# Kernel tuning notes

Hardware: AMD Instinct MI355X
Metric: run time of the kernel (lower is better)

## Reference

```python
import jax, jax.numpy as jnp
import numpy as np

N = 50000      # nodes
E = 800000     # edges
F = 64         # in_channels == out_channels
ED = 16        # edge_dim
G = 64         # graphs in batch
L = 2          # numLayers
BN_EPS = 1e-5
STD_EPS = 1e-5
AGG_DIM = F * 4 * 3  # 4 aggregators x 3 scalers


def setup_inputs() -> dict:
    key = jax.random.key(0)
    ks = jax.random.split(key, 12)
    r = lambda k, shp, fan: (jax.random.normal(k, shp, jnp.float32) / np.sqrt(fan)).astype(jnp.float32)
    return dict(
        x=jax.random.normal(ks[0], (N, F), jnp.float32),
        edge_attr=jax.random.normal(ks[1], (E, ED), jnp.float32),
        We=r(ks[2], (L, ED, F), ED), be=jnp.zeros((L, F), jnp.float32),
        Wpre=r(ks[3], (L, 3 * F, F), 3 * F), bpre=jnp.zeros((L, F), jnp.float32),
        Wpost=r(ks[4], (L, F + AGG_DIM, F), F + AGG_DIM), bpost=jnp.zeros((L, F), jnp.float32),
        Wlin=r(ks[5], (L, F, F), F), blin=jnp.zeros((L, F), jnp.float32),
        gamma=jnp.ones((L, F), jnp.float32), beta=jnp.zeros((L, F), jnp.float32),
        W1=r(ks[6], (F, 40), F), b1=jnp.zeros((40,), jnp.float32),
        W2=r(ks[7], (40, 1), 40), b2=jnp.zeros((1,), jnp.float32),
        edge_index=jax.random.randint(ks[8], (2, E), 0, N),
        batch=jnp.sort(jax.random.randint(ks[9], (N,), 0, G)),
    )


def _ceal_conv(x, src, dst, edge_attr, We, be, Wpre, bpre, Wpost, bpost, Wlin, blin, deg, amp, att):
    # PNA-style conv, towers=1, pre_layers=post_layers=1
    e = edge_attr @ We + be                                              # [E,F]
    h = jnp.concatenate([x[dst], x[src], e], axis=-1) @ Wpre + bpre      # [E,F]
    degc = jnp.maximum(deg, 1.0)[:, None]
    mean = jax.ops.segment_sum(h, dst, num_segments=N) / degc
    sq = jax.ops.segment_sum(h * h, dst, num_segments=N) / degc
    std = jnp.sqrt(jax.nn.relu(sq - mean * mean) + STD_EPS)
    has = (deg > 0)[:, None]
    mn = jnp.where(has, jax.ops.segment_min(h, dst, num_segments=N), 0.0)
    mx = jnp.where(has, jax.ops.segment_max(h, dst, num_segments=N), 0.0)
    aggs = jnp.concatenate([mean, mn, mx, std], axis=-1)                 # [N,4F]
    scaled = jnp.concatenate([aggs, aggs * amp[:, None], aggs * att[:, None]], axis=-1)  # [N,12F]
    out = jnp.concatenate([x, scaled], axis=-1) @ Wpost + bpost          # [N,F]
    return out @ Wlin + blin


def _bn(x, gamma, beta):
    mu = x.mean(0)
    var = x.var(0)  # biased, as torch BatchNorm training-mode normalization
    return (x - mu) * jax.lax.rsqrt(var + BN_EPS) * gamma + beta


def reference(x, edge_attr, We, be, Wpre, bpre, Wpost, bpost, Wlin, blin,
              gamma, beta, W1, b1, W2, b2, edge_index, batch):
    src, dst = edge_index[0], edge_index[1]
    deg = jax.ops.segment_sum(jnp.ones((E,), jnp.float32), dst, num_segments=N)
    avg_log = jnp.mean(jnp.log(deg + 1.0))
    logd = jnp.log(jnp.maximum(deg, 1.0) + 1.0)
    amp = logd / avg_log
    att = avg_log / logd
    for l in range(L):
        x = _ceal_conv(x, src, dst, edge_attr, We[l], be[l], Wpre[l], bpre[l],
                       Wpost[l], bpost[l], Wlin[l], blin[l], deg, amp, att)
        x = jax.nn.relu(_bn(x, gamma[l], beta[l]))
    cnt = jnp.maximum(jax.ops.segment_sum(jnp.ones((N,), jnp.float32), batch, num_segments=G), 1.0)
    gm = jax.ops.segment_sum(x, batch, num_segments=G) / cnt[:, None]    # global_mean_pool [G,F]
    return jax.nn.relu(gm @ W1 + b1) @ W2 + b2                           # [G,1]
```

## Files before the change

### kernel.cpp

```cpp
#include <hip/hip_runtime.h>
#include <math.h>
#include <float.h>

#define NN 50000
#define EE 800000
#define FF 64
#define EDIM 16
#define GG 64
#define NB64 782
#define NSB 196

typedef short bf16x8 __attribute__((ext_vector_type(8)));
typedef float f32x4 __attribute__((ext_vector_type(4)));

__device__ inline unsigned short bf_rne(float v) {
  unsigned int u = __float_as_uint(v);
  unsigned int r = (u + 0x7FFFu + ((u >> 16) & 1u)) >> 16;
  return (unsigned short)r;
}
__device__ inline float bf_up(unsigned short h) {
  return __uint_as_float(((unsigned int)h) << 16);
}
__device__ inline void split4(float4 v, ushort4& h, ushort4& l) {
  h.x = bf_rne(v.x); h.y = bf_rne(v.y); h.z = bf_rne(v.z); h.w = bf_rne(v.w);
  l.x = bf_rne(v.x - bf_up(h.x));
  l.y = bf_rne(v.y - bf_up(h.y));
  l.z = bf_rne(v.z - bf_up(h.z));
  l.w = bf_rne(v.w - bf_up(h.w));
}
__device__ inline float blo(unsigned int u) { return __uint_as_float(u << 16); }
__device__ inline float bhi(unsigned int u) { return __uint_as_float(u & 0xFFFF0000u); }

__global__ void k_deg(const int* __restrict__ eidx, int* __restrict__ deg) {
  int e = blockIdx.x * 256 + threadIdx.x;
  if (e < EE) atomicAdd(&deg[eidx[EE + e]], 1);
}

__global__ __launch_bounds__(256) void k_scanA(const int* __restrict__ deg, int* __restrict__ offsets,
                                               int* __restrict__ bsum, float* __restrict__ lsum) {
  __shared__ int ws[4];
  __shared__ float lw[4];
  int t = threadIdx.x;
  int lane = t & 63;
  int wv = t >> 6;
  int i = blockIdx.x * 256 + t;
  int v = (i < NN) ? deg[i] : 0;
  float lg = (i < NN) ? logf((float)v + 1.0f) : 0.0f;
  int x = v;
  #pragma unroll
  for (int o = 1; o < 64; o <<= 1) {
    int y = __shfl_up(x, o);
    if (lane >= o) x += y;
  }
  #pragma unroll
  for (int o = 1; o < 64; o <<= 1) lg += __shfl_xor(lg, o);
  if (lane == 63) ws[wv] = x;
  if (lane == 0) lw[wv] = lg;
  __syncthreads();
  int pre = 0;
  for (int k = 0; k < wv; k++) pre += ws[k];
  if (i < NN) offsets[i] = pre + x - v;
  if (t == 0) {
    bsum[blockIdx.x] = ws[0] + ws[1] + ws[2] + ws[3];
    lsum[blockIdx.x] = lw[0] + lw[1] + lw[2] + lw[3];
  }
}

__global__ __launch_bounds__(256) void k_scanB(const int* __restrict__ bsum, const float* __restrict__ lsum,
                                               int* __restrict__ bpref, float* __restrict__ meta,
                                               float* __restrict__ scbA) {
  __shared__ int ws[4];
  __shared__ float lw[4];
  int t = threadIdx.x;
  int lane = t & 63;
  int wv = t >> 6;
  int v = (t < NSB) ? bsum[t] : 0;
  float lg = (t < NSB) ? lsum[t] : 0.0f;
  int x = v;
  #pragma unroll
  for (int o = 1; o < 64; o <<= 1) {
    int y = __shfl_up(x, o);
    if (lane >= o) x += y;
  }
  #pragma unroll
  for (int o = 1; o < 64; o <<= 1) lg += __shfl_xor(lg, o);
  if (lane == 63) ws[wv] = x;
  if (lane == 0) lw[wv] = lg;
  __syncthreads();
  int pre = 0;
  for (int k = 0; k < wv; k++) pre += ws[k];
  if (t < NSB) bpref[t] = pre + x - v;
  if (t == 0) meta[0] = (lw[0] + lw[1] + lw[2] + lw[3]) / (float)NN;
  if (t < 64) { scbA[t] = 1.0f; scbA[64 + t] = 0.0f; }
  if (t == 0) scbA[128] = -FLT_MAX;
}

__global__ __launch_bounds__(256) void k_scanC(int* __restrict__ offsets, const int* __restrict__ bpref,
                                               const int* __restrict__ deg, const float* __restrict__ meta,
                                               float* __restrict__ amp, float* __restrict__ att) {
  int i = blockIdx.x * 256 + threadIdx.x;
  if (i < NN) {
    offsets[i] += bpref[blockIdx.x];
    float d = (float)deg[i];
    float avg = meta[0];
    float logd = logf(fmaxf(d, 1.0f) + 1.0f);
    amp[i] = logd / avg;
    att[i] = avg / logd;
  }
  if (i == 0) offsets[NN] = EE;
}

__global__ void k_scatter(const int* __restrict__ eidx, const int* __restrict__ offsets,
                          int* __restrict__ cursor, int* __restrict__ srcs,
                          const float* __restrict__ eattr, unsigned int* __restrict__ PermEA) {
  int e = blockIdx.x * 256 + threadIdx.x;
  if (e < EE) {
    int s = eidx[e];
    int d = eidx[EE + e];
    int pos = offsets[d] + atomicAdd(&cursor[d], 1);
    srcs[pos] = s;
    const float4* ep = (const float4*)(eattr + (size_t)e * EDIM);
    float4 q0 = ep[0], q1 = ep[1], q2 = ep[2], q3 = ep[3];
    uint4 pa, pb;
    pa.x = (unsigned)bf_rne(q0.x) | ((unsigned)bf_rne(q0.y) << 16);
    pa.y = (unsigned)bf_rne(q0.z) | ((unsigned)bf_rne(q0.w) << 16);
    pa.z = (unsigned)bf_rne(q1.x) | ((unsigned)bf_rne(q1.y) << 16);
    pa.w = (unsigned)bf_rne(q1.z) | ((unsigned)bf_rne(q1.w) << 16);
    pb.x = (unsigned)bf_rne(q2.x) | ((unsigned)bf_rne(q2.y) << 16);
    pb.y = (unsigned)bf_rne(q2.z) | ((unsigned)bf_rne(q2.w) << 16);
    pb.z = (unsigned)bf_rne(q3.x) | ((unsigned)bf_rne(q3.y) << 16);
    pb.w = (unsigned)bf_rne(q3.z) | ((unsigned)bf_rne(q3.w) << 16);
    ((uint4*)PermEA)[(size_t)pos * 2] = pa;
    ((uint4*)PermEA)[(size_t)pos * 2 + 1] = pb;
  }
}

__global__ __launch_bounds__(256) void k_prep2(const float* __restrict__ We, const float* __restrict__ be,
                                               const float* __restrict__ Wpre, const float* __restrict__ bpre,
                                               const float* __restrict__ Wpost, const float* __restrict__ bpost,
                                               const float* __restrict__ Wlin, const float* __restrict__ blin,
                                               unsigned short* __restrict__ MwT_h, unsigned short* __restrict__ MwT_l,
                                               float* __restrict__ bconst,
                                               unsigned short* __restrict__ WcT_h, unsigned short* __restrict__ WcT_l,
                                               unsigned short* __restrict__ WxT_h, unsigned short* __restrict__ WxT_l,
                                               float* __restrict__ bcomb) {
  int id = blockIdx.x * 256 + threadIdx.x;
  if (id < 53248) {
    int k = id >> 6, f = id & 63;
    float a = 0.0f;
    for (int j = 0; j < FF; j++) a += Wpost[(size_t)k * FF + j] * Wlin[j * FF + f];
    unsigned short h = bf_rne(a);
    WcT_h[f * 832 + k] = h;
    WcT_l[f * 832 + k] = bf_rne(a - bf_up(h));
  } else if (id < 61440) {
    int lid = id - 53248;
    int j = lid >> 6, k = lid & 63;
    float v = (j < 64) ? Wpre[k * FF + j] : Wpre[(64 + k) * FF + (j - 64)];
    unsigned short h = bf_rne(v);
    WxT_h[j * 64 + k] = h;
    WxT_l[j * 64 + k] = bf_rne(v - bf_up(h));
  } else if (id < 62464) {
    int lid = id - 61440;
    int k = lid >> 6, f = lid & 63;
    float a = 0.0f;
    for (int j = 0; j < FF; j++) a += We[k * FF + j] * Wpre[(128 + j) * FF + f];
    unsigned short h = bf_rne(a);
    int ct = f & 3, jcol = f >> 2;
    MwT_h[(ct * 16 + jcol) * 16 + k] = h;
    MwT_l[(ct * 16 + jcol) * 16 + k] = bf_rne(a - bf_up(h));
  } else {
    int f = threadIdx.x;
    if (blockIdx.x == 244 && f < 64) {
      float b = bpre[f];
      for (int j = 0; j < FF; j++) b += be[j] * Wpre[(128 + j) * FF + f];
      bconst[f] = b;
      float c = blin[f];
      for (int j = 0; j < FF; j++) c += bpost[j] * Wlin[j * FF + f];
      bcomb[f] = c;
    }
  }
}

__global__ __launch_bounds__(256) void k_xform(const float* __restrict__ x, const float* __restrict__ scb,
                                               const unsigned short* __restrict__ WxT_h,
                                               const unsigned short* __restrict__ WxT_l,
                                               float* __restrict__ Xd, unsigned short* __restrict__ Xs) {
  __shared__ unsigned short Ah[64 * 72], Al[64 * 72];
  int t = threadIdx.x;
  int n0 = blockIdx.x * 64;
  {
    int r = t >> 2, c0 = (t & 3) * 16;
    int n = n0 + r;
    bool rok = n < NN;
    const float4* src = (const float4*)(x + (size_t)n * FF + c0);
    float flr = scb[128];
    #pragma unroll
    for (int c4 = 0; c4 < 4; c4++) {
      float4 v = rok ? src[c4] : make_float4(0.f, 0.f, 0.f, 0.f);
      float4 sc = ((const float4*)scb)[(c0 >> 2) + c4];
      float4 of = ((const float4*)(scb + 64))[(c0 >> 2) + c4];
      v.x = fmaxf(v.x * sc.x + of.x, flr);
      v.y = fmaxf(v.y * sc.y + of.y, flr);
      v.z = fmaxf(v.z * sc.z + of.z, flr);
      v.w = fmaxf(v.w * sc.w + of.w, flr);
      ushort4 h4, l4;
      split4(v, h4, l4);
      *(ushort4*)&Ah[r * 72 + c0 + c4 * 4] = h4;
      *(ushort4*)&Al[r * 72 + c0 + c4 * 4] = l4;
    }
  }
  __syncthreads();
  int lane = t & 63;
  int l15 = lane & 15;
  int quad = lane >> 4;
  int w = __builtin_amdgcn_readfirstlane(t >> 6);
  int rbase = (w & 1) * 32;
  int cbase = (w >> 1) * 64;
  f32x4 acc[2][4];
  #pragma unroll
  for (int rt = 0; rt < 2; rt++)
    #pragma unroll
    for (int ct = 0; ct < 4; ct++) acc[rt][ct] = (f32x4){0.f, 0.f, 0.f, 0.f};

  #pragma unroll
  for (int ks = 0; ks < 2; ks++) {
    bf16x8 a_h[2], a_l[2];
    #pragma unroll
    for (int rt = 0; rt < 2; rt++) {
      int row = rbase + rt * 16 + l15;
      a_h[rt] = *(const bf16x8*)&Ah[row * 72 + ks * 32 + quad * 8];
      a_l[rt] = *(const bf16x8*)&Al[row * 72 + ks * 32 + quad * 8];
    }
    #pragma unroll
    for (int ct = 0; ct < 4; ct++) {
      int col = cbase + ct * 16 + l15;
      bf16x8 b_h = *(const bf16x8*)(WxT_h + (size_t)col * 64 + ks * 32 + quad * 8);
      bf16x8 b_l = *(const bf16x8*)(WxT_l + (size_t)col * 64 + ks * 32 + quad * 8);
      #pragma unroll
      for (int rt = 0; rt < 2; rt++) {
        acc[rt][ct] = __builtin_amdgcn_mfma_f32_16x16x32_bf16(a_h[rt], b_h, acc[rt][ct], 0, 0, 0);
        acc[rt][ct] = __builtin_amdgcn_mfma_f32_16x16x32_bf16(a_h[rt], b_l, acc[rt][ct], 0, 0, 0);
        acc[rt][ct] = __builtin_amdgcn_mfma_f32_16x16x32_bf16(a_l[rt], b_h, acc[rt][ct], 0, 0, 0);
      }
    }
  }
  #pragma unroll
  for (int rt = 0; rt < 2; rt++) {
    #pragma unroll
    for (int ct = 0; ct < 4; ct++) {
      int col = cbase + ct * 16 + l15;
      #pragma unroll
      for (int reg = 0; reg < 4; reg++) {
        int n = n0 + rbase + rt * 16 + quad * 4 + reg;
        if (n < NN) {
          float v = acc[rt][ct][reg];
          if (col < 64) Xd[(size_t)n * FF + col] = v;
          else          Xs[(size_t)n * FF + (col - 64)] = bf_rne(v);
        }
      }
    }
  }
}

__global__ __launch_bounds__(256) void k_agg(const int* __restrict__ srcs, const int* __restrict__ offsets,
                                             const unsigned int* __restrict__ PermEA,
                                             const unsigned short* __restrict__ MwT_h,
                                             const unsigned short* __restrict__ MwT_l,
                                             const float* __restrict__ bconst,
                                             const float* __restrict__ Xd, const unsigned short* __restrict__ Xs,
                                             unsigned short* __restrict__ aggs) {
  int wid = __builtin_amdgcn_readfirstlane(threadIdx.x >> 6);
  int lane = threadIdx.x & 63;
  int l15 = lane & 15;
  int quad = lane >> 4;
  int n = blockIdx.x * 4 + wid;
  if (n >= NN) return;

  bf16x8 bh[4], bl[4];
  #pragma unroll
  for (int ct = 0; ct < 4; ct++) {
    if (quad < 2) {
      bh[ct] = *(const bf16x8*)&MwT_h[(ct * 16 + l15) * 16 + quad * 8];
      bl[ct] = *(const bf16x8*)&MwT_l[(ct * 16 + l15) * 16 + quad * 8];
    } else {
      bh[ct] = (bf16x8){0, 0, 0, 0, 0, 0, 0, 0};
      bl[ct] = (bf16x8){0, 0, 0, 0, 0, 0, 0, 0};
    }
  }

  float4 xd4 = *(const float4*)(Xd + (size_t)n * FF + 4 * l15);
  float4 bc4 = *(const float4*)(bconst + 4 * l15);
  float bas[4] = {xd4.x + bc4.x, xd4.y + bc4.y, xd4.z + bc4.z, xd4.w + bc4.w};

  int o0 = offsets[n], o1 = offsets[n + 1];
  float s[4]  = {0.f, 0.f, 0.f, 0.f};
  float sq[4] = {0.f, 0.f, 0.f, 0.f};
  float mn[4] = {FLT_MAX, FLT_MAX, FLT_MAX, FLT_MAX};
  float mx[4] = {-FLT_MAX, -FLT_MAX, -FLT_MAX, -FLT_MAX};

  for (int base = o0; base < o1; base += 16) {
    bf16x8 af = (bf16x8){0, 0, 0, 0, 0, 0, 0, 0};
    if (quad < 2) af = *(const bf16x8*)(PermEA + (size_t)(base + l15) * 8 + quad * 4);
    f32x4 acc[4];
    #pragma unroll
    for (int ct = 0; ct < 4; ct++) {
      f32x4 a = (f32x4){0.f, 0.f, 0.f, 0.f};
      a = __builtin_amdgcn_mfma_f32_16x16x32_bf16(af, bl[ct], a, 0, 0, 0);
      a = __builtin_amdgcn_mfma_f32_16x16x32_bf16(af, bh[ct], a, 0, 0, 0);
      acc[ct] = a;
    }
    #pragma unroll
    for (int reg = 0; reg < 4; reg++) {
      int e = base + quad * 4 + reg;
      bool valid = e < o1;
      int ec = min(e, o1 - 1);
      int src = srcs[ec];
      ushort4 xs4 = *(const ushort4*)(Xs + (size_t)src * FF + 4 * l15);
      float xf[4] = {bf_up(xs4.x), bf_up(xs4.y), bf_up(xs4.z), bf_up(xs4.w)};
      #pragma unroll
      for (int ct = 0; ct < 4; ct++) {
        float h = bas[ct] + xf[ct] + acc[ct][reg];
        float hv = valid ? h : 0.0f;
        s[ct] += hv;
        sq[ct] = fmaf(hv, hv, sq[ct]);
        float t1 = fminf(mn[ct], h);
        float t2 = fmaxf(mx[ct], h);
        mn[ct] = valid ? t1 : mn[ct];
        mx[ct] = valid ? t2 : mx[ct];
      }
    }
  }

  #pragma unroll
  for (int ct = 0; ct < 4; ct++) {
    s[ct] += __shfl_xor(s[ct], 16);  s[ct] += __shfl_xor(s[ct], 32);
    sq[ct] += __shfl_xor(sq[ct], 16); sq[ct] += __shfl_xor(sq[ct], 32);
    mn[ct] = fminf(mn[ct], __shfl_xor(mn[ct], 16)); mn[ct] = fminf(mn[ct], __shfl_xor(mn[ct], 32));
    mx[ct] = fmaxf(mx[ct], __shfl_xor(mx[ct], 16)); mx[ct] = fmaxf(mx[ct], __shfl_xor(mx[ct], 32));
  }

  float d = (float)(o1 - o0);
  float dc = fmaxf(d, 1.0f);
  float rdc = 1.0f / dc;
  bool has = d > 0.0f;
  ushort4 outv;
  unsigned short ov[4];
  #pragma unroll
  for (int ct = 0; ct < 4; ct++) {
    float mean = s[ct] * rdc;
    float msq = sq[ct] * rdc;
    float sd = sqrtf(fmaxf(msq - mean * mean, 0.0f) + 1e-5f);
    float vmn = has ? mn[ct] : 0.0f;
    float vmx = has ? mx[ct] : 0.0f;
    float val = (quad == 0) ? mean : (quad == 1) ? vmn : (quad == 2) ? vmx : sd;
    ov[ct] = bf_rne(val);
  }
  outv.x = ov[0]; outv.y = ov[1]; outv.z = ov[2]; outv.w = ov[3];
  *(ushort4*)(aggs + (size_t)n * 256 + quad * 64 + 4 * l15) = outv;
}

__global__ __launch_bounds__(256) void k_post(const float* __restrict__ x, const float* __restrict__ scb,
                                              const unsigned short* __restrict__ aggs,
                                              const float* __restrict__ amp, const float* __restrict__ att,
                                              const unsigned short* __restrict__ WcT_h,
                                              const unsigned short* __restrict__ WcT_l,
                                              const float* __restrict__ bcomb,
                                              float* __restrict__ y, float* __restrict__ partials) {
  __shared__ unsigned short Ah[64 * 72], Al[64 * 72];
  __shared__ float red_s[4][32], red_q[4][32];
  int t = threadIdx.x;
  int n0 = blockIdx.x * 64;
  int lane = t & 63;
  int l15 = lane & 15;
  int quad = lane >> 4;
  int w = __builtin_amdgcn_readfirstlane(t >> 6);
  int rbase = (w & 1) * 32;
  int cbase = (w >> 1) * 32;

  {
    int ar = t >> 2;
    int ac0 = (t & 3) * 16;
    int an = n0 + ar;
    bool rok = an < NN;
    const float* xrow = x + (size_t)an * FF;
    float flr = scb[128];
    #pragma unroll
    for (int c4 = 0; c4 < 4; c4++) {
      float4 v = rok ? *(const float4*)(xrow + ac0 + c4 * 4) : make_float4(0.f, 0.f, 0.f, 0.f);
      float4 sc = ((const float4*)scb)[(ac0 >> 2) + c4];
      float4 of = ((const float4*)(scb + 64))[(ac0 >> 2) + c4];
      v.x = fmaxf(v.x * sc.x + of.x, flr);
      v.y = fmaxf(v.y * sc.y + of.y, flr);
      v.z = fmaxf(v.z * sc.z + of.z, flr);
      v.w = fmaxf(v.w * sc.w + of.w, flr);
      ushort4 h4, l4;
      split4(v, h4, l4);
      *(ushort4*)&Ah[ar * 72 + ac0 + c4 * 4] = h4;
      *(ushort4*)&Al[ar * 72 + ac0 + c4 * 4] = l4;
    }
  }
  __syncthreads();

  f32x4 acc[3][2][2];
  #pragma unroll
  for (int s = 0; s < 3; s++)
    #pragma unroll
    for (int rt = 0; rt < 2; rt++)
      #pragma unroll
      for (int ct = 0; ct < 2; ct++) acc[s][rt][ct] = (f32x4){0.f, 0.f, 0.f, 0.f};

  #pragma unroll
  for (int ks = 0; ks < 2; ks++) {
    bf16x8 a_h[2], a_l[2];
    #pragma unroll
    for (int rt = 0; rt < 2; rt++) {
      int row = rbase + rt * 16 + l15;
      a_h[rt] = *(const bf16x8*)&Ah[row * 72 + ks * 32 + quad * 8];
      a_l[rt] = *(const bf16x8*)&Al[row * 72 + ks * 32 + quad * 8];
    }
    #pragma unroll
    for (int ct = 0; ct < 2; ct++) {
      int col = cbase + ct * 16 + l15;
      bf16x8 b_h = *(const bf16x8*)(WcT_h + (size_t)col * 832 + ks * 32 + quad * 8);
      bf16x8 b_l = *(const bf16x8*)(WcT_l + (size_t)col * 832 + ks * 32 + quad * 8);
      #pragma unroll
      for (int rt = 0; rt < 2; rt++) {
        acc[0][rt][ct] = __builtin_amdgcn_mfma_f32_16x16x32_bf16(a_h[rt], b_h, acc[0][rt][ct], 0, 0, 0);
        acc[0][rt][ct] = __builtin_amdgcn_mfma_f32_16x16x32_bf16(a_h[rt], b_l, acc[0][rt][ct], 0, 0, 0);
        acc[0][rt][ct] = __builtin_amdgcn_mfma_f32_16x16x32_bf16(a_l[rt], b_h, acc[0][rt][ct], 0, 0, 0);
      }
    }
  }

  #pragma unroll
  for (int c = 0; c < 4; c++) {
    #pragma unroll
    for (int ks = 0; ks < 2; ks++) {
      bf16x8 a[2];
      #pragma unroll
      for (int rt = 0; rt < 2; rt++) {
        int row = n0 + rbase + rt * 16 + l15;
        row = min(row, NN - 1);
        a[rt] = *(const bf16x8*)(aggs + (size_t)row * 256 + c * 64 + ks * 32 + quad * 8);
      }
      #pragma unroll
      for (int s = 0; s < 3; s++) {
        int kb = 64 + s * 256 + c * 64 + ks * 32 + quad * 8;
        #pragma unroll
        for (int ct = 0; ct < 2; ct++) {
          int col = cbase + ct * 16 + l15;
          bf16x8 b_h = *(const bf16x8*)(WcT_h + (size_t)col * 832 + kb);
          bf16x8 b_l = *(const bf16x8*)(WcT_l + (size_t)col * 832 + kb);
          #pragma unroll
          for (int rt = 0; rt < 2; rt++) {
            acc[s][rt][ct] = __builtin_amdgcn_mfma_f32_16x16x32_bf16(a[rt], b_h, acc[s][rt][ct], 0, 0, 0);
            acc[s][rt][ct] = __builtin_amdgcn_mfma_f32_16x16x32_bf16(a[rt], b_l, acc[s][rt][ct], 0, 0, 0);
          }
        }
      }
    }
  }

  float ps[2] = {0.f, 0.f}, pq[2] = {0.f, 0.f};
  float bc[2];
  #pragma unroll
  for (int ct = 0; ct < 2; ct++) bc[ct] = bcomb[cbase + ct * 16 + l15];
  #pragma unroll
  for (int rt = 0; rt < 2; rt++) {
    #pragma unroll
    for (int reg = 0; reg < 4; reg++) {
      int n = n0 + rbase + rt * 16 + quad * 4 + reg;
      bool ok = n < NN;
      int nc = min(n, NN - 1);
      float am = amp[nc];
      float at = att[nc];
      #pragma unroll
      for (int ct = 0; ct < 2; ct++) {
        float v = acc[0][rt][ct][reg] + am * acc[1][rt][ct][reg] + at * acc[2][rt][ct][reg] + bc[ct];
        if (ok) {
          y[(size_t)n * FF + (cbase + ct * 16 + l15)] = v;
          ps[ct] += v;
          pq[ct] += v * v;
        }
      }
    }
  }
  #pragma unroll
  for (int ct = 0; ct < 2; ct++) {
    ps[ct] += __shfl_xor(ps[ct], 16);
    ps[ct] += __shfl_xor(ps[ct], 32);
    pq[ct] += __shfl_xor(pq[ct], 16);
    pq[ct] += __shfl_xor(pq[ct], 32);
  }
  if (quad == 0) {
    #pragma unroll
    for (int ct = 0; ct < 2; ct++) {
      red_s[w][ct * 16 + l15] = ps[ct];
      red_q[w][ct * 16 + l15] = pq[ct];
    }
  }
  __syncthreads();
  if (t < 64) {
    float ss, qq;
    if (t < 32) { ss = red_s[0][t] + red_s[1][t]; qq = red_q[0][t] + red_q[1][t]; }
    else        { ss = red_s[2][t - 32] + red_s[3][t - 32]; qq = red_q[2][t - 32] + red_q[3][t - 32]; }
    partials[(size_t)blockIdx.x * 128 + t] = ss;
    partials[(size_t)blockIdx.x * 128 + 64 + t] = qq;
  }
}

__global__ __launch_bounds__(1024) void k_bnfin(const float* __restrict__ partials,
                                                const float* __restrict__ gamma, const float* __restrict__ beta,
                                                float* __restrict__ scb) {
  __shared__ float red[1024];
  __shared__ double tot[128];
  int t = threadIdx.x;
  int c = t & 127, seg = t >> 7;
  float s = 0.f;
  for (int i = seg; i < NB64; i += 8) s += partials[(size_t)i * 128 + c];
  red[t] = s;
  __syncthreads();
  if (t < 128) {
    double d = 0.0;
    #pragma unroll
    for (int sg = 0; sg < 8; sg++) d += (double)red[sg * 128 + t];
    tot[t] = d;
  }
  __syncthreads();
  if (t < 64) {
    double mu = tot[t] / (double)NN;
    double var = tot[64 + t] / (double)NN - mu * mu;
    float sc = gamma[t] * rsqrtf((float)fmax(var, 0.0) + 1e-5f);
    scb[t] = sc;
    scb[64 + t] = beta[t] - (float)mu * sc;
  }
  if (t == 0) scb[128] = 0.0f;
}

__global__ __launch_bounds__(256) void k_pool(const float* __restrict__ x, const float* __restrict__ scb,
                                              const int* __restrict__ batch,
                                              float* __restrict__ psum, float* __restrict__ cnt) {
  int lane = threadIdx.x & 63;
  int wv = threadIdx.x >> 6;
  int wglobal = blockIdx.x * 4 + wv;
  int nw = gridDim.x * 4;
  int per = (NN + nw - 1) / nw;
  int n0 = wglobal * per;
  int n1 = min(n0 + per, NN);
  if (n0 >= n1) return;
  float sc = scb[lane], of = scb[64 + lane], flr = scb[128];
  int gcur = batch[n0];
  float acc = 0.0f;
  int count = 0;
  for (int n = n0; n < n1; n++) {
    int g = batch[n];
    float v = fmaxf(x[(size_t)n * FF + lane] * sc + of, flr);
    if (g != gcur) {
      atomicAdd(&psum[gcur * FF + lane], acc);
      if (lane == 0) atomicAdd(&cnt[gcur], (float)count);
      gcur = g; acc = 0.0f; count = 0;
    }
    acc += v;
    count++;
  }
  atomicAdd(&psum[gcur * FF + lane], acc);
  if (lane == 0) atomicAdd(&cnt[gcur], (float)count);
}

__global__ void k_final(const float* __restrict__ psum, const float* __restrict__ cnt,
                        const float* __restrict__ W1, const float* __restrict__ b1,
                        const float* __restrict__ W2, const float* __restrict__ b2, float* __restrict__ out) {
  int g = threadIdx.x;
  if (g >= GG) return;
  float c = fmaxf(cnt[g], 1.0f);
  float gm[64];
  #pragma unroll
  for (int i = 0; i < 64; i++) gm[i] = psum[g * FF + i] / c;
  float o = b2[0];
  for (int h = 0; h < 40; h++) {
    float a = b1[h];
    #pragma unroll
    for (int i = 0; i < 64; i++) a += gm[i] * W1[i * 40 + h];
    o += fmaxf(a, 0.0f) * W2[h];
  }
  out[g] = o;
}

extern "C" void kernel_launch(void* const* d_in, const int* in_sizes, int n_in,
                              void* d_out, int out_size, void* d_ws, size_t ws_size,
                              hipStream_t stream) {
  (void)in_sizes; (void)n_in; (void)out_size; (void)ws_size;
  const float* x0    = (const float*)d_in[0];
  const float* eattr = (const float*)d_in[1];
  const float* We    = (const float*)d_in[2];
  const float* be    = (const float*)d_in[3];
  const float* Wpre  = (const float*)d_in[4];
  const float* bpre  = (const float*)d_in[5];
  const float* Wpost = (const float*)d_in[6];
  const float* bpost = (const float*)d_in[7];
  const float* Wlin  = (const float*)d_in[8];
  const float* blin  = (const float*)d_in[9];
  const float* gamma = (const float*)d_in[10];
  const float* beta  = (const float*)d_in[11];
  const float* W1    = (const float*)d_in[12];
  const float* b1    = (const float*)d_in[13];
  const float* W2    = (const float*)d_in[14];
  const float* b2    = (const float*)d_in[15];
  const int* eidx    = (const int*)d_in[16];
  const int* batch   = (const int*)d_in[17];
  float* out = (float*)d_out;

  char* w = (char*)d_ws;
  size_t off = 0;
  auto alloc = [&](size_t bytes) -> void* {
    void* p = w + off;
    off += bytes;
    off = (off + 255) & ~(size_t)255;
    return p;
  };
  int*    deg     = (int*)alloc(NN * sizeof(int));
  int*    offsets = (int*)alloc((NN + 1) * sizeof(int));
  int*    cursor  = (int*)alloc(NN * sizeof(int));
  int*    srcs    = (int*)alloc((EE + 16) * sizeof(int));
  unsigned int* PermEA = (unsigned int*)alloc(((size_t)EE + 16) * 8 * sizeof(unsigned int));
  int*    bsum    = (int*)alloc(NSB * sizeof(int));
  int*    bpref   = (int*)alloc(NSB * sizeof(int));
  float*  lsum    = (float*)alloc(NSB * sizeof(float));
  float*  meta    = (float*)alloc(sizeof(float));
  float*  amp     = (float*)alloc(NN * sizeof(float));
  float*  att     = (float*)alloc(NN * sizeof(float));
  unsigned short* MwT_h = (unsigned short*)alloc(FF * EDIM * sizeof(unsigned short));
  unsigned short* MwT_l = (unsigned short*)alloc(FF * EDIM * sizeof(unsigned short));
  float*  bconst  = (float*)alloc(FF * sizeof(float));
  float*  bcomb   = (float*)alloc(FF * sizeof(float));
  float*  scbA    = (float*)alloc(129 * sizeof(float));
  float*  scbB    = (float*)alloc(2 * 129 * sizeof(float));
  unsigned short* WcT_h = (unsigned short*)alloc(FF * 832 * sizeof(unsigned short));
  unsigned short* WcT_l = (unsigned short*)alloc(FF * 832 * sizeof(unsigned short));
  unsigned short* WxT_h = (unsigned short*)alloc(128 * 64 * sizeof(unsigned short));
  unsigned short* WxT_l = (unsigned short*)alloc(128 * 64 * sizeof(unsigned short));
  float*  partials = (float*)alloc((size_t)NB64 * 128 * sizeof(float));
  float*  Xd      = (float*)alloc((size_t)NN * FF * sizeof(float));
  unsigned short* Xs = (unsigned short*)alloc((size_t)NN * FF * sizeof(unsigned short));
  unsigned short* aggs = (unsigned short*)alloc((size_t)NN * 256 * sizeof(unsigned short));
  float*  ybuf    = (float*)alloc((size_t)NN * FF * sizeof(float));
  float*  psum    = (float*)alloc((GG * FF + GG) * sizeof(float));
  float*  cnt     = psum + GG * FF;

  hipMemsetAsync(deg, 0, NN * sizeof(int), stream);
  hipMemsetAsync(cursor, 0, NN * sizeof(int), stream);
  hipMemsetAsync(srcs + EE, 0, 16 * sizeof(int), stream);
  hipMemsetAsync(psum, 0, (GG * FF + GG) * sizeof(float), stream);

  k_deg<<<(EE + 255) / 256, 256, 0, stream>>>(eidx, deg);
  k_scanA<<<NSB, 256, 0, stream>>>(deg, offsets, bsum, lsum);
  k_scanB<<<1, 256, 0, stream>>>(bsum, lsum, bpref, meta, scbA);
  k_scanC<<<NSB, 256, 0, stream>>>(offsets, bpref, deg, meta, amp, att);
  k_scatter<<<(EE + 255) / 256, 256, 0, stream>>>(eidx, offsets, cursor, srcs, eattr, PermEA);

  const float* xin = x0;
  const float* scb_in = scbA;
  for (int l = 0; l < 2; l++) {
    k_prep2<<<245, 256, 0, stream>>>(We + l * EDIM * FF, be + l * FF, Wpre + (size_t)l * 3 * FF * FF,
                                     bpre + l * FF, Wpost + (size_t)l * 832 * FF, bpost + l * FF,
                                     Wlin + l * FF * FF, blin + l * FF,
                                     MwT_h, MwT_l, bconst, WcT_h, WcT_l, WxT_h, WxT_l, bcomb);
    k_xform<<<NB64, 256, 0, stream>>>(xin, scb_in, WxT_h, WxT_l, Xd, Xs);
    k_agg<<<(NN + 3) / 4, 256, 0, stream>>>(srcs, offsets, PermEA, MwT_h, MwT_l, bconst, Xd, Xs, aggs);
    k_post<<<NB64, 256, 0, stream>>>(xin, scb_in, aggs, amp, att, WcT_h, WcT_l, bcomb, ybuf, partials);
    k_bnfin<<<1, 1024, 0, stream>>>(partials, gamma + l * FF, beta + l * FF, scbB + l * 129);
    xin = ybuf;
    scb_in = scbB + l * 129;
  }
  k_pool<<<200, 256, 0, stream>>>(ybuf, scbB + 129, batch, psum, cnt);
  k_final<<<1, 64, 0, stream>>>(psum, cnt, W1, b1, W2, b2, out);
}
```

Baseline: 608.5 us.

## Stage GEMM weights in LDS, batch weight prep, replace memsets with kernel

The xform and post kernels now copy their bf16 hi/lo weight tiles into shared memory and feed the MFMAs from LDS instead of reading global memory per wave. The post kernel also stages the aggregate rows through LDS, chunk by chunk, with barriers between chunks. Weight preprocessing for both layers is merged into one launch before the layer loop, and the four memsets become a single zero-fill kernel. These changes target redundant global weight loads and launch overhead, at the cost of more LDS use, which may lower occupancy, and extra synchronisation in k_post.

New measurement: 527.2 us. 1.15x faster.

```diff
diff --git a/kernel.cpp b/kernel.cpp
--- a/kernel.cpp
+++ b/kernel.cpp
@@ -28,8 +28,14 @@
   l.z = bf_rne(v.z - bf_up(h.z));
   l.w = bf_rne(v.w - bf_up(h.w));
 }
-__device__ inline float blo(unsigned int u) { return __uint_as_float(u << 16); }
-__device__ inline float bhi(unsigned int u) { return __uint_as_float(u & 0xFFFF0000u); }
+
+__global__ __launch_bounds__(256) void k_zfill(int* __restrict__ deg, int* __restrict__ cursor,
+                                               int* __restrict__ srcs_slack, float* __restrict__ psum) {
+  int i = blockIdx.x * 256 + threadIdx.x;
+  if (i < NN) { deg[i] = 0; cursor[i] = 0; }
+  if (i < 16) srcs_slack[i] = 0;
+  if (i < GG * FF + GG) psum[i] = 0.0f;
+}
 
 __global__ void k_deg(const int* __restrict__ eidx, int* __restrict__ deg) {
   int e = blockIdx.x * 256 + threadIdx.x;
@@ -144,7 +150,18 @@
                                                unsigned short* __restrict__ WcT_h, unsigned short* __restrict__ WcT_l,
                                                unsigned short* __restrict__ WxT_h, unsigned short* __restrict__ WxT_l,
                                                float* __restrict__ bcomb) {
-  int id = blockIdx.x * 256 + threadIdx.x;
+  int layer = blockIdx.x / 245;
+  int blk = blockIdx.x % 245;
+  We += (size_t)layer * EDIM * FF;  be += layer * FF;
+  Wpre += (size_t)layer * 3 * FF * FF; bpre += layer * FF;
+  Wpost += (size_t)layer * 832 * FF; bpost += layer * FF;
+  Wlin += (size_t)layer * FF * FF; blin += layer * FF;
+  MwT_h += layer * 1024; MwT_l += layer * 1024;
+  bconst += layer * FF; bcomb += layer * FF;
+  WcT_h += (size_t)layer * 53248; WcT_l += (size_t)layer * 53248;
+  WxT_h += layer * 8192; WxT_l += layer * 8192;
+
+  int id = blk * 256 + threadIdx.x;
   if (id < 53248) {
     int k = id >> 6, f = id & 63;
     float a = 0.0f;
@@ -170,7 +187,7 @@
     MwT_l[(ct * 16 + jcol) * 16 + k] = bf_rne(a - bf_up(h));
   } else {
     int f = threadIdx.x;
-    if (blockIdx.x == 244 && f < 64) {
+    if (blk == 244 && f < 64) {
       float b = bpre[f];
       for (int j = 0; j < FF; j++) b += be[j] * Wpre[(128 + j) * FF + f];
       bconst[f] = b;
@@ -186,8 +203,19 @@
                                                const unsigned short* __restrict__ WxT_l,
                                                float* __restrict__ Xd, unsigned short* __restrict__ Xs) {
   __shared__ unsigned short Ah[64 * 72], Al[64 * 72];
+  __shared__ unsigned short Bh[128 * 72], Bl[128 * 72];
   int t = threadIdx.x;
   int n0 = blockIdx.x * 64;
+  {
+    int j = t >> 1, half = t & 1;
+    const ushort4* srch = (const ushort4*)(WxT_h + j * 64 + half * 32);
+    const ushort4* srcl = (const ushort4*)(WxT_l + j * 64 + half * 32);
+    #pragma unroll
+    for (int i = 0; i < 8; i++) {
+      *(ushort4*)&Bh[j * 72 + half * 32 + i * 4] = srch[i];
+      *(ushort4*)&Bl[j * 72 + half * 32 + i * 4] = srcl[i];
+    }
+  }
   {
     int r = t >> 2, c0 = (t & 3) * 16;
     int n = n0 + r;
@@ -234,8 +262,8 @@
     #pragma unroll
     for (int ct = 0; ct < 4; ct++) {
       int col = cbase + ct * 16 + l15;
-      bf16x8 b_h = *(const bf16x8*)(WxT_h + (size_t)col * 64 + ks * 32 + quad * 8);
-      bf16x8 b_l = *(const bf16x8*)(WxT_l + (size_t)col * 64 + ks * 32 + quad * 8);
+      bf16x8 b_h = *(const bf16x8*)&Bh[col * 72 + ks * 32 + quad * 8];
+      bf16x8 b_l = *(const bf16x8*)&Bl[col * 72 + ks * 32 + quad * 8];
       #pragma unroll
       for (int rt = 0; rt < 2; rt++) {
         acc[rt][ct] = __builtin_amdgcn_mfma_f32_16x16x32_bf16(a_h[rt], b_h, acc[rt][ct], 0, 0, 0);
@@ -367,6 +395,7 @@
                                               const float* __restrict__ bcomb,
                                               float* __restrict__ y, float* __restrict__ partials) {
   __shared__ unsigned short Ah[64 * 72], Al[64 * 72];
+  __shared__ unsigned short Bh[64 * 72], Bl[64 * 72];
   __shared__ float red_s[4][32], red_q[4][32];
   int t = threadIdx.x;
   int n0 = blockIdx.x * 64;
@@ -377,13 +406,23 @@
   int rbase = (w & 1) * 32;
   int cbase = (w >> 1) * 32;
 
+  int ar = t >> 2;
+  int ac0 = (t & 3) * 16;
+  int an = n0 + ar;
+  bool rok = an < NN;
+  const float* xrow = x + (size_t)an * FF;
+  const unsigned short* arow = aggs + (size_t)an * 256;
+  float flr = scb[128];
+
+  f32x4 acc[3][2][2];
+  #pragma unroll
+  for (int s = 0; s < 3; s++)
+    #pragma unroll
+    for (int rt = 0; rt < 2; rt++)
+      #pragma unroll
+      for (int ct = 0; ct < 2; ct++) acc[s][rt][ct] = (f32x4){0.f, 0.f, 0.f, 0.f};
+
   {
-    int ar = t >> 2;
-    int ac0 = (t & 3) * 16;
-    int an = n0 + ar;
-    bool rok = an < NN;
-    const float* xrow = x + (size_t)an * FF;
-    float flr = scb[128];
     #pragma unroll
     for (int c4 = 0; c4 < 4; c4++) {
       float4 v = rok ? *(const float4*)(xrow + ac0 + c4 * 4) : make_float4(0.f, 0.f, 0.f, 0.f);
@@ -398,66 +437,85 @@
       *(ushort4*)&Ah[ar * 72 + ac0 + c4 * 4] = h4;
       *(ushort4*)&Al[ar * 72 + ac0 + c4 * 4] = l4;
     }
-  }
-  __syncthreads();
-
-  f32x4 acc[3][2][2];
-  #pragma unroll
-  for (int s = 0; s < 3; s++)
-    #pragma unroll
-    for (int rt = 0; rt < 2; rt++)
-      #pragma unroll
-      for (int ct = 0; ct < 2; ct++) acc[s][rt][ct] = (f32x4){0.f, 0.f, 0.f, 0.f};
-
-  #pragma unroll
-  for (int ks = 0; ks < 2; ks++) {
-    bf16x8 a_h[2], a_l[2];
-    #pragma unroll
-    for (int rt = 0; rt < 2; rt++) {
-      int row = rbase + rt * 16 + l15;
-      a_h[rt] = *(const bf16x8*)&Ah[row * 72 + ks * 32 + quad * 8];
-      a_l[rt] = *(const bf16x8*)&Al[row * 72 + ks * 32 + quad * 8];
-    }
-    #pragma unroll
-    for (int ct = 0; ct < 2; ct++) {
-      int col = cbase + ct * 16 + l15;
-      bf16x8 b_h = *(const bf16x8*)(WcT_h + (size_t)col * 832 + ks * 32 + quad * 8);
-      bf16x8 b_l = *(const bf16x8*)(WcT_l + (size_t)col * 832 + ks * 32 + quad * 8);
+    const ushort4* sh = (const ushort4*)(WcT_h + ar * 832 + ac0);
+    const ushort4* sl = (const ushort4*)(WcT_l + ar * 832 + ac0);
+    #pragma unroll
+    for (int i = 0; i < 4; i++) {
+      *(ushort4*)&Bh[ar * 72 + ac0 + i * 4] = sh[i];
+      *(ushort4*)&Bl[ar * 72 + ac0 + i * 4] = sl[i];
+    }
+    __syncthreads();
+    #pragma unroll
+    for (int ks = 0; ks < 2; ks++) {
+      bf16x8 a_h[2], a_l[2], b_h[2], b_l[2];
       #pragma unroll
       for (int rt = 0; rt < 2; rt++) {
-        acc[0][rt][ct] = __builtin_amdgcn_mfma_f32_16x16x32_bf16(a_h[rt], b_h, acc[0][rt][ct], 0, 0, 0);
-        acc[0][rt][ct] = __builtin_amdgcn_mfma_f32_16x16x32_bf16(a_h[rt], b_l, acc[0][rt][ct], 0, 0, 0);
-        acc[0][rt][ct] = __builtin_amdgcn_mfma_f32_16x16x32_bf16(a_l[rt], b_h, acc[0][rt][ct], 0, 0, 0);
-      }
-    }
-  }
-
-  #pragma unroll
+        int row = rbase + rt * 16 + l15;
+        a_h[rt] = *(const bf16x8*)&Ah[row * 72 + ks * 32 + quad * 8];
+        a_l[rt] = *(const bf16x8*)&Al[row * 72 + ks * 32 + quad * 8];
+      }
+      #pragma unroll
+      for (int ct = 0; ct < 2; ct++) {
+        int col = cbase + ct * 16 + l15;
+        b_h[ct] = *(const bf16x8*)&Bh[col * 72 + ks * 32 + quad * 8];
+        b_l[ct] = *(const bf16x8*)&Bl[col * 72 + ks * 32 + quad * 8];
+      }
+      #pragma unroll
+      for (int rt = 0; rt < 2; rt++)
+        #pragma unroll
+        for (int ct = 0; ct < 2; ct++) {
+          acc[0][rt][ct] = __builtin_amdgcn_mfma_f32_16x16x32_bf16(a_h[rt], b_h[ct], acc[0][rt][ct], 0, 0, 0);
+          acc[0][rt][ct] = __builtin_amdgcn_mfma_f32_16x16x32_bf16(a_h[rt], b_l[ct], acc[0][rt][ct], 0, 0, 0);
+          acc[0][rt][ct] = __builtin_amdgcn_mfma_f32_16x16x32_bf16(a_l[rt], b_h[ct], acc[0][rt][ct], 0, 0, 0);
+        }
+    }
+    __syncthreads();
+  }
+
   for (int c = 0; c < 4; c++) {
     #pragma unroll
-    for (int ks = 0; ks < 2; ks++) {
-      bf16x8 a[2];
-      #pragma unroll
-      for (int rt = 0; rt < 2; rt++) {
-        int row = n0 + rbase + rt * 16 + l15;
-        row = min(row, NN - 1);
-        a[rt] = *(const bf16x8*)(aggs + (size_t)row * 256 + c * 64 + ks * 32 + quad * 8);
-      }
-      #pragma unroll
-      for (int s = 0; s < 3; s++) {
-        int kb = 64 + s * 256 + c * 64 + ks * 32 + quad * 8;
+    for (int s = 0; s < 3; s++) {
+      if (s == 0) {
+        #pragma unroll
+        for (int c4 = 0; c4 < 4; c4++) {
+          ushort4 u = rok ? *(const ushort4*)(arow + c * 64 + ac0 + c4 * 4) : make_ushort4(0, 0, 0, 0);
+          *(ushort4*)&Ah[ar * 72 + ac0 + c4 * 4] = u;
+        }
+      }
+      {
+        int kbase = 64 + s * 256 + c * 64;
+        const ushort4* sh = (const ushort4*)(WcT_h + ar * 832 + kbase + ac0);
+        const ushort4* sl = (const ushort4*)(WcT_l + ar * 832 + kbase + ac0);
+        #pragma unroll
+        for (int i = 0; i < 4; i++) {
+          *(ushort4*)&Bh[ar * 72 + ac0 + i * 4] = sh[i];
+          *(ushort4*)&Bl[ar * 72 + ac0 + i * 4] = sl[i];
+        }
+      }
+      __syncthreads();
+      #pragma unroll
+      for (int ks = 0; ks < 2; ks++) {
+        bf16x8 a[2], b_h[2], b_l[2];
+        #pragma unroll
+        for (int rt = 0; rt < 2; rt++) {
+          int row = rbase + rt * 16 + l15;
+          a[rt] = *(const bf16x8*)&Ah[row * 72 + ks * 32 + quad * 8];
+        }
         #pragma unroll
         for (int ct = 0; ct < 2; ct++) {
           int col = cbase + ct * 16 + l15;
-          bf16x8 b_h = *(const bf16x8*)(WcT_h + (size_t)col * 832 + kb);
-          bf16x8 b_l = *(const bf16x8*)(WcT_l + (size_t)col * 832 + kb);
+          b_h[ct] = *(const bf16x8*)&Bh[col * 72 + ks * 32 + quad * 8];
+          b_l[ct] = *(const bf16x8*)&Bl[col * 72 + ks * 32 + quad * 8];
+        }
+        #pragma unroll
+        for (int rt = 0; rt < 2; rt++)
           #pragma unroll
-          for (int rt = 0; rt < 2; rt++) {
-            acc[s][rt][ct] = __builtin_amdgcn_mfma_f32_16x16x32_bf16(a[rt], b_h, acc[s][rt][ct], 0, 0, 0);
-            acc[s][rt][ct] = __builtin_amdgcn_mfma_f32_16x16x32_bf16(a[rt], b_l, acc[s][rt][ct], 0, 0, 0);
+          for (int ct = 0; ct < 2; ct++) {
+            acc[s][rt][ct] = __builtin_amdgcn_mfma_f32_16x16x32_bf16(a[rt], b_h[ct], acc[s][rt][ct], 0, 0, 0);
+            acc[s][rt][ct] = __builtin_amdgcn_mfma_f32_16x16x32_bf16(a[rt], b_l[ct], acc[s][rt][ct], 0, 0, 0);
           }
-        }
-      }
+      }
+      __syncthreads();
     }
   }
 
@@ -629,16 +687,16 @@
   float*  meta    = (float*)alloc(sizeof(float));
   float*  amp     = (float*)alloc(NN * sizeof(float));
   float*  att     = (float*)alloc(NN * sizeof(float));
-  unsigned short* MwT_h = (unsigned short*)alloc(FF * EDIM * sizeof(unsigned short));
-  unsigned short* MwT_l = (unsigned short*)alloc(FF * EDIM * sizeof(unsigned short));
-  float*  bconst  = (float*)alloc(FF * sizeof(float));
-  float*  bcomb   = (float*)alloc(FF * sizeof(float));
+  unsigned short* MwT_h = (unsigned short*)alloc(2 * FF * EDIM * sizeof(unsigned short));
+  unsigned short* MwT_l = (unsigned short*)alloc(2 * FF * EDIM * sizeof(unsigned short));
+  float*  bconst  = (float*)alloc(2 * FF * sizeof(float));
+  float*  bcomb   = (float*)alloc(2 * FF * sizeof(float));
   float*  scbA    = (float*)alloc(129 * sizeof(float));
   float*  scbB    = (float*)alloc(2 * 129 * sizeof(float));
-  unsigned short* WcT_h = (unsigned short*)alloc(FF * 832 * sizeof(unsigned short));
-  unsigned short* WcT_l = (unsigned short*)alloc(FF * 832 * sizeof(unsigned short));
-  unsigned short* WxT_h = (unsigned short*)alloc(128 * 64 * sizeof(unsigned short));
-  unsigned short* WxT_l = (unsigned short*)alloc(128 * 64 * sizeof(unsigned short));
+  unsigned short* WcT_h = (unsigned short*)alloc(2 * (size_t)FF * 832 * sizeof(unsigned short));
+  unsigned short* WcT_l = (unsigned short*)alloc(2 * (size_t)FF * 832 * sizeof(unsigned short));
+  unsigned short* WxT_h = (unsigned short*)alloc(2 * 128 * 64 * sizeof(unsigned short));
+  unsigned short* WxT_l = (unsigned short*)alloc(2 * 128 * 64 * sizeof(unsigned short));
   float*  partials = (float*)alloc((size_t)NB64 * 128 * sizeof(float));
   float*  Xd      = (float*)alloc((size_t)NN * FF * sizeof(float));
   unsigned short* Xs = (unsigned short*)alloc((size_t)NN * FF * sizeof(unsigned short));
@@ -647,27 +705,24 @@
   float*  psum    = (float*)alloc((GG * FF + GG) * sizeof(float));
   float*  cnt     = psum + GG * FF;
 
-  hipMemsetAsync(deg, 0, NN * sizeof(int), stream);
-  hipMemsetAsync(cursor, 0, NN * sizeof(int), stream);
-  hipMemsetAsync(srcs + EE, 0, 16 * sizeof(int), stream);
-  hipMemsetAsync(psum, 0, (GG * FF + GG) * sizeof(float), stream);
-
+  k_zfill<<<NSB, 256, 0, stream>>>(deg, cursor, srcs + EE, psum);
   k_deg<<<(EE + 255) / 256, 256, 0, stream>>>(eidx, deg);
   k_scanA<<<NSB, 256, 0, stream>>>(deg, offsets, bsum, lsum);
   k_scanB<<<1, 256, 0, stream>>>(bsum, lsum, bpref, meta, scbA);
   k_scanC<<<NSB, 256, 0, stream>>>(offsets, bpref, deg, meta, amp, att);
   k_scatter<<<(EE + 255) / 256, 256, 0, stream>>>(eidx, offsets, cursor, srcs, eattr, PermEA);
+  k_prep2<<<490, 256, 0, stream>>>(We, be, Wpre, bpre, Wpost, bpost, Wlin, blin,
+                                   MwT_h, MwT_l, bconst, WcT_h, WcT_l, WxT_h, WxT_l, bcomb);
 
   const float* xin = x0;
   const float* scb_in = scbA;
   for (int l = 0; l < 2; l++) {
-    k_prep2<<<245, 256, 0, stream>>>(We + l * EDIM * FF, be + l * FF, Wpre + (size_t)l * 3 * FF * FF,
-                                     bpre + l * FF, Wpost + (size_t)l * 832 * FF, bpost + l * FF,
-                                     Wlin + l * FF * FF, blin + l * FF,
-                                     MwT_h, MwT_l, bconst, WcT_h, WcT_l, WxT_h, WxT_l, bcomb);
-    k_xform<<<NB64, 256, 0, stream>>>(xin, scb_in, WxT_h, WxT_l, Xd, Xs);
-    k_agg<<<(NN + 3) / 4, 256, 0, stream>>>(srcs, offsets, PermEA, MwT_h, MwT_l, bconst, Xd, Xs, aggs);
-    k_post<<<NB64, 256, 0, stream>>>(xin, scb_in, aggs, amp, att, WcT_h, WcT_l, bcomb, ybuf, partials);
+    k_xform<<<NB64, 256, 0, stream>>>(xin, scb_in, WxT_h + l * 8192, WxT_l + l * 8192, Xd, Xs);
+    k_agg<<<(NN + 3) / 4, 256, 0, stream>>>(srcs, offsets, PermEA, MwT_h + l * 1024, MwT_l + l * 1024,
+                                            bconst + l * FF, Xd, Xs, aggs);
+    k_post<<<NB64, 256, 0, stream>>>(xin, scb_in, aggs, amp, att,
+                                     WcT_h + (size_t)l * 53248, WcT_l + (size_t)l * 53248,
+                                     bcomb + l * FF, ybuf, partials);
     k_bnfin<<<1, 1024, 0, stream>>>(partials, gamma + l * FF, beta + l * FF, scbB + l * 129);
     xin = ybuf;
     scb_in = scbB + l * 129;
```
